# Optimization experiments

Hardware: AMD Instinct MI355X
Metric: run time of the kernel (lower is better)

The kernel has to match this reference:

```python
import jax, jax.numpy as jnp
import numpy as np

B, NJ, NW, NT, D, H = 1024, 16, 2, 2, 128, 128


def _mlp2(x, W1, b1, W2, b2):
    # two-layer dense net with relu on every layer (edge/node networks)
    return jax.nn.relu(jax.nn.relu(x @ W1 + b1) @ W2 + b2)


def _edge_block(src, dst, W1, b1, W2, b2, mask_dst=None):
    # fully-connected edge block: edge(i,j) = MLP(concat(src_i, dst_j)),
    # then avg-pool over destination nodes (masked if mask_dst given)
    Bb, Ns, ds = src.shape
    Nd, dd = dst.shape[1], dst.shape[2]
    e_in = jnp.concatenate([
        jnp.broadcast_to(src[:, :, None, :], (Bb, Ns, Nd, ds)),
        jnp.broadcast_to(dst[:, None, :, :], (Bb, Ns, Nd, dd)),
    ], axis=-1)                              # [B, Ns, Nd, 2D]
    h = _mlp2(e_in, W1, b1, W2, b2)          # [B, Ns, Nd, H]
    if mask_dst is not None:
        m = mask_dst.astype(h.dtype)[:, None, :, None]
        pooled = (h * m).sum(axis=2) / jnp.maximum(m.sum(axis=2), 1.0)
    else:
        pooled = h.mean(axis=2)
    return pooled                            # [B, Ns, H]


def setup_inputs() -> dict:
    key = jax.random.key(0)
    ks = jax.random.split(key, 10)
    def w(k, shape, fan_in):
        return jax.random.normal(k, shape, jnp.float32) / np.float32(np.sqrt(fan_in))
    return {
        "jets": jax.random.normal(ks[0], (B, NJ, D), jnp.float32),
        "nodes_w": jax.random.normal(ks[1], (B, NW, D), jnp.float32),
        "nodes_top": jax.random.normal(ks[2], (B, NT, D), jnp.float32),
        "mask": jax.random.bernoulli(ks[3], 0.8, (B, NJ)),
        # 7 edge nets: 0 jet-jet, 1 jet-W, 2 jet-top, 3 W-jet, 4 W-top, 5 top-jet, 6 top-W
        "edge_W1": w(ks[4], (7, 2 * D, H), 2 * D),
        "edge_b1": jnp.zeros((7, H), jnp.float32),
        "edge_W2": w(ks[5], (7, H, H), H),
        "edge_b2": jnp.zeros((7, H), jnp.float32),
        # jet node net: input D + 3H
        "jet_W1": w(ks[6], (D + 3 * H, H), D + 3 * H),
        "jet_b1": jnp.zeros((H,), jnp.float32),
        "jet_W2": w(ks[7], (H, H), H),
        "jet_b2": jnp.zeros((H,), jnp.float32),
        # W / top node nets (stacked): input D + 2H
        "wt_W1": w(ks[8], (2, D + 2 * H, H), D + 2 * H),
        "wt_b1": jnp.zeros((2, H), jnp.float32),
        "wt_W2": w(ks[9], (2, H, H), H),
        "wt_b2": jnp.zeros((2, H), jnp.float32),
    }


def reference(jets, nodes_w, nodes_top, mask,
              edge_W1, edge_b1, edge_W2, edge_b2,
              jet_W1, jet_b1, jet_W2, jet_b2,
              wt_W1, wt_b1, wt_W2, wt_b2):
    eb = lambda i, s, d, m: _edge_block(s, d, edge_W1[i], edge_b1[i], edge_W2[i], edge_b2[i], m)
    mf = mask.astype(jets.dtype)
    # --- jet update ---
    p_jj = eb(0, jets, jets, mask)
    p_jw = eb(1, jets, nodes_w, None)
    p_jt = eb(2, jets, nodes_top, None)
    jets_cat = jnp.concatenate([jets, p_jj, p_jw, p_jt], axis=-1)
    jets_out = _mlp2(jets_cat, jet_W1, jet_b1, jet_W2, jet_b2) * mf[..., None]
    # --- W update ---
    p_wj = eb(3, nodes_w, jets, mask)
    p_wt = eb(4, nodes_w, nodes_top, None)
    ws_out = _mlp2(jnp.concatenate([nodes_w, p_wj, p_wt], axis=-1),
                   wt_W1[0], wt_b1[0], wt_W2[0], wt_b2[0])
    # --- top update ---
    p_tj = eb(5, nodes_top, jets, mask)
    p_tw = eb(6, nodes_top, nodes_w, None)
    tops_out = _mlp2(jnp.concatenate([nodes_top, p_tj, p_tw], axis=-1),
                     wt_W1[1], wt_b1[1], wt_W2[1], wt_b2[1])
    # concat all updated node types along the node axis: [B, NJ+NW+NT, H]
    return jnp.concatenate([jets_out, ws_out, tops_out], axis=1)
```

## Files before the change

kernel.cpp:

```cpp
#include <hip/hip_runtime.h>
#include <hip/hip_bf16.h>


using short4v = __attribute__((ext_vector_type(4))) short;
using short8 = __attribute__((ext_vector_type(8))) short;
using f32x4  = __attribute__((ext_vector_type(4))) float;
using u32x4  = __attribute__((ext_vector_type(4))) unsigned;

#define DEVI __device__ __forceinline__

DEVI float b2f(short s){
  unsigned u = ((unsigned)(unsigned short)s) << 16;
  float f; __builtin_memcpy(&f, &u, 4); return f;
}
DEVI float lo16f(unsigned w){ unsigned u = w << 16; float f; __builtin_memcpy(&f,&u,4); return f; }
DEVI float hi16f(unsigned w){ unsigned u = w & 0xffff0000u; float f; __builtin_memcpy(&f,&u,4); return f; }
DEVI short f2b(float f){
  __hip_bfloat16 h = __float2bfloat16(f);
  short s; __builtin_memcpy(&s, &h, 2); return s;
}
DEVI unsigned cvtpk(float lo, float hi){
  unsigned r;
  asm("v_cvt_pk_bf16_f32 %0, %1, %2" : "=v"(r) : "v"(lo), "v"(hi));
  return r;
}
DEVI float ldflex(const void* p, long i, int bf){
  return bf ? b2f(((const short*)p)[i]) : ((const float*)p)[i];
}
DEVI f32x4 mfma16(short8 a, short8 b, f32x4 c){
  return __builtin_amdgcn_mfma_f32_16x16x32_bf16(a, b, c, 0, 0, 0);
}

DEVI int detect_bf(const void* jets){
  int l = threadIdx.x & 63;
  int extreme = 0;
  #pragma unroll
  for(int s=0;s<4;s++){
    unsigned short v = ((const unsigned short*)jets)[(l*4+s)*2];
    int e = (v>>7)&0xff;
    if(e<110||e>140) extreme++;
  }
  #pragma unroll
  for(int o=1;o<64;o<<=1) extreme += __shfl_xor(extreme, o);
  return (extreme <= 32) ? 1 : 0;
}
DEVI int detect_fmt(const void* mask){
  int l = threadIdx.x & 63;
  bool all01=true, allf32=true;
  #pragma unroll
  for(int s=0;s<4;s++){
    unsigned w = ((const unsigned*)mask)[l*4+s];
    if(w>1u) all01=false;
    if(w!=0u && w!=0x3F800000u) allf32=false;
  }
  bool allbfv=true; int evnz=0;
  #pragma unroll
  for(int s=0;s<8;s++){
    unsigned short v = ((const unsigned short*)mask)[l*8+s];
    if(v!=0&&v!=0x3F80) allbfv=false;
    if(((l*8+s)&1)==0 && v!=0) evnz++;
  }
  #pragma unroll
  for(int o=1;o<64;o<<=1) evnz += __shfl_xor(evnz, o);
  bool allb01=true;
  #pragma unroll
  for(int s=0;s<16;s++){ if(((const unsigned char*)mask)[l*16+s]>1) allb01=false; }
  int a01 = __all(all01), af32 = __all(allf32), abf = __all(allbfv), ab01 = __all(allb01);
  int fmt = 0;
  if(a01) fmt=0; else if(abf && evnz>0) fmt=2; else if(af32) fmt=3; else if(ab01) fmt=1;
  return fmt;
}

constexpr size_t OF_MASKF  = 256;
constexpr size_t OF_INVCNT = 65792;
constexpr size_t OF_XJ     = 69888;
constexpr size_t OF_XW     = 4264192;
constexpr size_t OF_XT     = 4788480;
constexpr size_t OF_W1T    = 5312768;
constexpr size_t OF_W2T    = 5771520;
constexpr size_t OF_EB1F   = 6000896;
constexpr size_t OF_EB2F   = 6004480;
constexpr size_t OF_JW1T   = 6008064;
constexpr size_t OF_JW2T   = 6139136;
constexpr size_t OF_JB1F   = 6171904;
constexpr size_t OF_JB2F   = 6172416;
constexpr size_t OF_WTW1T  = 6172928;
constexpr size_t OF_WTW2T  = 6369536;
constexpr size_t OF_WTB1F  = 6435072;
constexpr size_t OF_WTB2F  = 6436096;
constexpr size_t OF_UVJ    = 6437120;
constexpr size_t OF_UVW    = 31602944;
constexpr size_t OF_UVT    = 33700096;
constexpr size_t OF_POOL   = 65157376;

__constant__ int QJ_NET[14]  = {0,0,1,2,3,5, 1,3,4,6, 2,4,5,6};
__constant__ int QJ_HALF[14] = {0,1,0,0,1,1, 1,0,0,1, 1,1,0,0};
__constant__ int EB_CUM[8] = {0,512,576,640,704,768,776,784};
__constant__ int EB_NET[7] = {0,1,2,3,5,4,6};
__constant__ int EN_LGRPB[7] = {8,5,5,5,2,5,2};
__constant__ int EN_LGND2[7] = {4,1,1,4,1,4,1};
__constant__ int EN_LGNSB[7] = {4,4,4,1,1,1,1};
__constant__ int EN_USEL[7] = {0,0,0,1,1,2,2};
__constant__ long long EN_UOFF[7] = {0,4194304,6291456,262144,524288,524288,786432};
__constant__ int EN_VSEL[7] = {0,1,2,0,2,0,1};
__constant__ long long EN_VOFF[7] = {2097152,0,0,8388608,262144,10485760,786432};
__constant__ long long EN_POOL[7] = {0,2097152,4194304,6291456,6553600,6815744,7077888};
__constant__ int TJ_CUM[21] = {0,32,64,96,128,160,192,224,240,256,272,288,304,320,336,400,416,464,512,528,544};
__constant__ int TJ_SEL[20] = {0,0,0,0,0,0,0,1,1,1,1,1,1,1,2,3,4,4,5,5};
__constant__ int TJ_OFF[20] = {0,32768,65536,98304,131072,163840,196608,
                               0,16384,32768,49152,65536,81920,98304,
                               0,0,0,49152,0,16384};
__constant__ int TJ_R[20]   = {256,256,256,256,256,256,256,128,128,128,128,128,128,128,512,128,384,384,128,128};

__global__ __launch_bounds__(256) void k_prep(
    const void* jets, const void* nw, const void* ntop, const void* mask,
    const void* eW1, const void* eb1, const void* eW2, const void* eb2,
    const void* jW1, const void* jb1, const void* jW2, const void* jb2,
    const void* wW1, const void* wb1, const void* wW2, const void* wb2,
    int* flags, float* maskf, float* invcnt,
    short* XJ, short* XW, short* XT,
    short* W1T, short* W2T, short* JW1T, short* JW2T, short* WTW1T, short* WTW2T,
    float* EB1F, float* EB2F, float* JB1F, float* JB2F, float* WTB1F, float* WTB2F){
  __shared__ float tl[32][33];
  int bid = blockIdx.x;
  if(bid < 2560){
    int bf = detect_bf(jets);
    long i = ((long)bid*256 + threadIdx.x)*4;
    const void* src; short* dst; long o;
    if(i < 2097152){ src=jets; dst=XJ; o=i; }
    else if(i < 2359296){ src=nw; dst=XW; o=i-2097152; }
    else { src=ntop; dst=XT; o=i-2359296; }
    short4v r;
    if(bf){
      r = *(const short4v*)((const short*)src + o);
    } else {
      f32x4 v = *(const f32x4*)((const float*)src + o);
      #pragma unroll
      for(int e=0;e<4;e++) r[e] = f2b(v[e]);
    }
    *(short4v*)(dst + o) = r;
  } else if(bid < 3104){
    int bf = detect_bf(jets);
    int tile = bid - 2560; int job = 0;
    while(tile >= TJ_CUM[job+1]) job++;
    tile -= TJ_CUM[job];
    int sel = TJ_SEL[job]; long off = TJ_OFF[job]; int R = TJ_R[job];
    const void* src = sel==0?eW1: sel==1?eW2: sel==2?jW1: sel==3?jW2: sel==4?wW1: wW2;
    short* dst = sel==0?W1T: sel==1?W2T: sel==2?JW1T: sel==3?JW2T: sel==4?WTW1T: WTW2T;
    int tr = (tile>>2)*32, tc = (tile&3)*32;
    int t = threadIdx.x, r = t>>3, c4 = (t&7)*4;
    #pragma unroll
    for(int j=0;j<4;j++) tl[r][c4+j] = ldflex(src, off + (long)(tr+r)*128 + tc + c4 + j, bf);
    __syncthreads();
    short4v o;
    #pragma unroll
    for(int j=0;j<4;j++) o[j] = f2b(tl[c4+j][r]);
    *(short4v*)(dst + off + (long)(tc+r)*R + tr + c4) = o;
  } else if(bid < 3168){
    int fmt = detect_fmt(mask);
    int t = (bid-3104)*256 + threadIdx.x;
    float m;
    if(fmt==0)      m = (((const int*)mask)[t]!=0) ? 1.f : 0.f;
    else if(fmt==1) m = (((const unsigned char*)mask)[t]!=0) ? 1.f : 0.f;
    else if(fmt==2) m = (b2f(((const short*)mask)[t])!=0.f) ? 1.f : 0.f;
    else            m = (((const float*)mask)[t]!=0.f) ? 1.f : 0.f;
    maskf[t] = m;
    float s = m;
    for(int o=1;o<16;o<<=1) s += __shfl_xor(s, o);
    if((t&15)==0) invcnt[t>>4] = 1.f / fmaxf(s, 1.f);
  } else if(bid < 3178){
    int bf = detect_bf(jets);
    int id = (bid-3168)*256 + threadIdx.x;
    if(id<896)        EB1F[id]       = ldflex(eb1, id, bf);
    else if(id<1792)  EB2F[id-896]   = ldflex(eb2, id-896, bf);
    else if(id<1920)  JB1F[id-1792]  = ldflex(jb1, id-1792, bf);
    else if(id<2048)  JB2F[id-1920]  = ldflex(jb2, id-1920, bf);
    else if(id<2304)  WTB1F[id-2048] = ldflex(wb1, id-2048, bf);
    else if(id<2560)  WTB2F[id-2304] = ldflex(wb2, id-2304, bf);
  } else {
    if(threadIdx.x < 64){
      int bf = detect_bf(jets);
      int fmt = detect_fmt(mask);
      if((threadIdx.x & 63) == 0){ flags[0] = bf; flags[1] = fmt; }
    }
  }
}

__global__ __launch_bounds__(512, 4) void k_proj(const short* XJ, const short* XW, const short* XT,
    const short* W1T, const float* EB1F, short* UVJ, short* UVW, short* UVT){
  int bid = blockIdx.x;
  int jp, rb; const short* X; short* out;
  if(bid < 384){ jp = bid>>6; rb = bid&63; X=XJ; out=UVJ + jp*2097152; }
  else if(bid < 416){ int r2=bid-384; jp = 6 + (r2>>3); rb = r2&7; X=XW; out=UVW + (jp-6)*262144; }
  else { int r2=bid-416; jp = 10 + (r2>>3); rb = r2&7; X=XT; out=UVT + (jp-10)*262144; }
  int net = QJ_NET[jp], half = QJ_HALF[jp];
  bool addb = (half==0);
  long row0 = (long)rb * 256;
  const short* Wb = W1T + net*32768 + half*128;
  int t = threadIdx.x, lane = t & 63, wv = t >> 6;
  int rbw = wv >> 1, ch = (wv & 1)*64;
  int cl = lane & 15, kh = lane >> 4;
  short8 bw[4][4];
  f32x4 biasv[4];
  #pragma unroll
  for(int nt=0;nt<4;nt++){
    #pragma unroll
    for(int ks=0;ks<4;ks++)
      bw[nt][ks] = *(const short8*)(Wb + (ch + nt*16 + cl)*256 + ks*32 + kh*8);
    if(addb) biasv[nt] = *(const f32x4*)(EB1F + net*128 + ch + nt*16 + kh*4);
    else     biasv[nt] = f32x4{0.f,0.f,0.f,0.f};
  }
  #pragma unroll 1
  for(int c=0;c<4;c++){
    long T0 = row0 + c*64 + rbw*16;
    short8 a[4];
    #pragma unroll
    for(int ks=0;ks<4;ks++)
      a[ks] = *(const short8*)(X + (T0 + cl)*128 + ks*32 + kh*8);
    f32x4 acc[4] = {};
    #pragma unroll
    for(int ks=0;ks<4;ks++)
      #pragma unroll
      for(int nt=0;nt<4;nt++)
        acc[nt] = mfma16(bw[nt][ks], a[ks], acc[nt]);
    #pragma unroll
    for(int nt=0;nt<4;nt++){
      short4v sv;
      #pragma unroll
      for(int r=0;r<4;r++) sv[r] = f2b(acc[nt][r] + biasv[nt][r]);
      *(short4v*)(out + (T0 + cl)*128 + ch + nt*16 + kh*4) = sv;
    }
  }
}

__global__ __launch_bounds__(512, 4) void k_edge(const short* UVJ, const short* UVW, const short* UVT,
    const short* W2T, const float* EB2F, const float* maskf, const float* invcnt, short* POOL){
  __shared__ short W2s[16384];
  int bid = blockIdx.x;
  int ni = 0;
  while(bid >= EB_CUM[ni+1]) ni++;
  int net = EB_NET[ni];
  long base = (long)(bid - EB_CUM[ni]) * 512;
  int t = threadIdx.x, lane = t & 63, wv = t >> 6;
  int cl = lane & 15, kh = lane >> 4;
  const short* Wg = W2T + net*16384;
  #pragma unroll
  for(int i2=0;i2<4;i2++){
    int c = t + i2*512;
    int row = c>>4, blk = c&15;
    u32x4 w4 = *(const u32x4*)(Wg + row*128 + blk*8);
    *(u32x4*)((char*)W2s + ((row*256 + blk*16) ^ ((row&7)<<4))) = w4;
  }
  int lgRPB = EN_LGRPB[net], lgNd = EN_LGND2[net], lgNsB = EN_LGNSB[net];
  int masked = (lgNd == 4);
  const short* U = (EN_USEL[net]==0?UVJ:(EN_USEL[net]==1?UVW:UVT)) + EN_UOFF[net];
  const short* V = (EN_VSEL[net]==0?UVJ:(EN_VSEL[net]==1?UVW:UVT)) + EN_VOFF[net];
  short* pool = POOL + EN_POOL[net];
  float bias[8];
  #pragma unroll
  for(int nt=0;nt<8;nt++) bias[nt] = EB2F[net*128 + nt*16 + cl];
  __syncthreads();
  for(int s=0;s<4;s++){
    long R0 = base + wv*64 + s*16;
    long e = R0 + cl;
    long urow = ((e>>lgRPB)<<lgNsB) + ((e & ((1<<lgRPB)-1)) >> lgNd);
    long vrow = ((e>>lgRPB)<<lgNd)  + (e & ((1<<lgNd)-1));
    u32x4 u[4], v[4];
    #pragma unroll
    for(int ks=0;ks<4;ks++){
      u[ks] = *(const u32x4*)(U + urow*128 + ks*32 + kh*8);
      v[ks] = *(const u32x4*)(V + vrow*128 + ks*32 + kh*8);
    }
    f32x4 acc[8];
    #pragma unroll
    for(int nt=0;nt<8;nt++) acc[nt] = f32x4{bias[nt],bias[nt],bias[nt],bias[nt]};
    #pragma unroll
    for(int ks=0;ks<4;ks++){
      u32x4 aw;
      #pragma unroll
      for(int p=0;p<4;p++){
        float al = fmaxf(lo16f(u[ks][p]) + lo16f(v[ks][p]), 0.f);
        float ah = fmaxf(hi16f(u[ks][p]) + hi16f(v[ks][p]), 0.f);
        aw[p] = cvtpk(al, ah);
      }
      short8 a = __builtin_bit_cast(short8, aw);
      #pragma unroll
      for(int nt=0;nt<8;nt++){
        int row = nt*16 + cl;
        short8 bb = *(const short8*)((const char*)W2s + ((row*256 + ks*64 + kh*16) ^ ((row&7)<<4)));
        acc[nt] = mfma16(a, bb, acc[nt]);
      }
    }
    if(masked){
      long b = R0 >> lgRPB;
      float ic = invcnt[b];
      float wr[4];
      #pragma unroll
      for(int r=0;r<4;r++) wr[r] = maskf[b*16 + kh*4 + r] * ic;
      long prow = R0 >> 4;
      #pragma unroll
      for(int nt=0;nt<8;nt++){
        int col = nt*16 + cl;
        float sm = fmaxf(acc[nt][0],0.f)*wr[0] + fmaxf(acc[nt][1],0.f)*wr[1]
                 + fmaxf(acc[nt][2],0.f)*wr[2] + fmaxf(acc[nt][3],0.f)*wr[3];
        sm += __shfl_xor(sm, 16);
        sm += __shfl_xor(sm, 32);
        if(lane < 16) pool[prow*128 + col] = f2b(sm);
      }
    } else {
      long pr = (R0 + kh*4) >> 1;
      #pragma unroll
      for(int nt=0;nt<8;nt++){
        int col = nt*16 + cl;
        float v0 = fmaxf(acc[nt][0],0.f), v1 = fmaxf(acc[nt][1],0.f);
        float v2 = fmaxf(acc[nt][2],0.f), v3 = fmaxf(acc[nt][3],0.f);
        pool[pr*128 + col]     = f2b((v0+v1)*0.5f);
        pool[(pr+1)*128 + col] = f2b((v2+v3)*0.5f);
      }
    }
  }
}

__global__ __launch_bounds__(256) void k_node(const short* XJ, const short* XW, const short* XT,
    const short* POOL, const short* JW1T, const short* JW2T, const float* JB1F, const float* JB2F,
    const short* WTW1T, const short* WTW2T, const float* WTB1F, const float* WTB2F,
    const float* maskf, const int* flags, void* out){
  __shared__ short hs[8192];
  int bid = blockIdx.x;
  int net; long row0;
  if(bid < 256){ net=0; row0=(long)bid*64; }
  else if(bid < 288){ net=1; row0=(long)(bid-256)*64; }
  else { net=2; row0=(long)(bid-288)*64; }
  int NQ = (net==0) ? 4 : 3;
  int K1 = NQ*128;
  const short* X = (net==0) ? XJ : ((net==1) ? XW : XT);
  const short *P1, *P2, *P3 = nullptr;
  if(net==0){ P1=POOL; P2=POOL+2097152; P3=POOL+4194304; }
  else if(net==1){ P1=POOL+6291456; P2=POOL+6553600; }
  else { P1=POOL+6815744; P2=POOL+7077888; }
  const short* W1 = (net==0) ? JW1T : WTW1T + (long)(net-1)*49152;
  const short* W2 = (net==0) ? JW2T : WTW2T + (long)(net-1)*16384;
  const float* B1 = (net==0) ? JB1F : WTB1F + (net-1)*128;
  const float* B2 = (net==0) ? JB2F : WTB2F + (net-1)*128;
  int t = threadIdx.x, lane = t & 63, wv = t >> 6;
  int cl = lane & 15, kh = lane >> 4;
  int rl = wv*16 + cl;
  long xrow = row0 + rl;
  f32x4 acc[8] = {};
  #pragma unroll
  for(int q=0;q<4;q++){
    if(q < NQ){
      const short* SA = (q==0)?X:((q==1)?P1:((q==2)?P2:P3));
      #pragma unroll
      for(int ks=0;ks<4;ks++){
        short8 a = *(const short8*)(SA + xrow*128 + ks*32 + kh*8);
        #pragma unroll
        for(int nt=0;nt<8;nt++){
          short8 bb = *(const short8*)(W1 + (long)(nt*16 + cl)*K1 + q*128 + ks*32 + kh*8);
          acc[nt] = mfma16(bb, a, acc[nt]);
        }
      }
    }
  }
  #pragma unroll
  for(int nt=0;nt<8;nt++){
    f32x4 bv = *(const f32x4*)(B1 + nt*16 + kh*4);
    short4v sv;
    #pragma unroll
    for(int r=0;r<4;r++) sv[r] = f2b(fmaxf(acc[nt][r] + bv[r], 0.f));
    *(short4v*)((char*)hs + ((rl*256 + (nt*16 + kh*4)*2) ^ ((rl&7)<<4))) = sv;
  }
  __syncthreads();
  f32x4 acc2[8] = {};
  #pragma unroll
  for(int k0=0;k0<4;k0++){
    short8 a = *(const short8*)((const char*)hs + ((rl*256 + (k0*32 + kh*8)*2) ^ ((rl&7)<<4)));
    #pragma unroll
    for(int nt=0;nt<8;nt++){
      short8 bb = *(const short8*)(W2 + (nt*16 + cl)*128 + k0*32 + kh*8);
      acc2[nt] = mfma16(bb, a, acc2[nt]);
    }
  }
  int obf = flags[0];
  long grow = row0 + rl;
  long bbn, node; float mscale = 1.f;
  if(net==0){ bbn = grow>>4; node = grow&15; mscale = maskf[grow]; }
  else if(net==1){ bbn = grow>>1; node = 16 + (grow&1); }
  else { bbn = grow>>1; node = 18 + (grow&1); }
  long obase = (bbn*20 + node)*128;
  #pragma unroll
  for(int nt=0;nt<8;nt++){
    f32x4 bv = *(const f32x4*)(B2 + nt*16 + kh*4);
    f32x4 fv;
    #pragma unroll
    for(int r=0;r<4;r++) fv[r] = fmaxf(acc2[nt][r] + bv[r], 0.f) * mscale;
    if(obf){
      short4v sv;
      #pragma unroll
      for(int r=0;r<4;r++) sv[r] = f2b(fv[r]);
      *(short4v*)((short*)out + obase + nt*16 + kh*4) = sv;
    } else {
      *(f32x4*)((float*)out + obase + nt*16 + kh*4) = fv;
    }
  }
}

extern "C" void kernel_launch(void* const* d_in, const int* in_sizes, int n_in,
                              void* d_out, int out_size, void* d_ws, size_t ws_size,
                              hipStream_t stream){
  char* ws = (char*)d_ws;
  int*   flags  = (int*)ws;
  float* maskf  = (float*)(ws + OF_MASKF);
  float* invcnt = (float*)(ws + OF_INVCNT);
  short* XJ     = (short*)(ws + OF_XJ);
  short* XW     = (short*)(ws + OF_XW);
  short* XT     = (short*)(ws + OF_XT);
  short* W1T    = (short*)(ws + OF_W1T);
  short* W2T    = (short*)(ws + OF_W2T);
  float* EB1F   = (float*)(ws + OF_EB1F);
  float* EB2F   = (float*)(ws + OF_EB2F);
  short* JW1T   = (short*)(ws + OF_JW1T);
  short* JW2T   = (short*)(ws + OF_JW2T);
  float* JB1F   = (float*)(ws + OF_JB1F);
  float* JB2F   = (float*)(ws + OF_JB2F);
  short* WTW1T  = (short*)(ws + OF_WTW1T);
  short* WTW2T  = (short*)(ws + OF_WTW2T);
  float* WTB1F  = (float*)(ws + OF_WTB1F);
  float* WTB2F  = (float*)(ws + OF_WTB2F);
  short* UVJ    = (short*)(ws + OF_UVJ);
  short* UVW    = (short*)(ws + OF_UVW);
  short* UVT    = (short*)(ws + OF_UVT);
  short* POOL   = (short*)(ws + OF_POOL);

  k_prep<<<3179, 256, 0, stream>>>(d_in[0], d_in[1], d_in[2], d_in[3],
                                   d_in[4], d_in[5], d_in[6], d_in[7],
                                   d_in[8], d_in[9], d_in[10], d_in[11],
                                   d_in[12], d_in[13], d_in[14], d_in[15],
                                   flags, maskf, invcnt, XJ, XW, XT,
                                   W1T, W2T, JW1T, JW2T, WTW1T, WTW2T,
                                   EB1F, EB2F, JB1F, JB2F, WTB1F, WTB2F);
  k_proj <<<448, 512, 0, stream>>>(XJ, XW, XT, W1T, EB1F, UVJ, UVW, UVT);
  k_edge <<<784, 512, 0, stream>>>(UVJ, UVW, UVT, W2T, EB2F, maskf, invcnt, POOL);
  k_node <<<320, 256, 0, stream>>>(XJ, XW, XT, POOL, JW1T, JW2T, JB1F, JB2F,
                                   WTW1T, WTW2T, WTB1F, WTB2F, maskf, flags, d_out);
}
```

Baseline: 121.4 us.

## Halve edge and node block work and restructure edge tile for B-fragment reuse

The edge kernel now has each block cover 256 edges instead of 512, doubling the grid. Each wave processes two 16-row tiles at once, so every W2 fragment read from LDS feeds two MFMAs, replacing a sequential four-step loop. The node kernel now uses 32-row blocks with waves split across output-column halves, doubling its grid. The aim is more blocks in flight and fewer LDS reads per MFMA, at the cost of reloading W2 into LDS twice as often and higher register pressure per wave.

```diff
diff --git a/kernel.cpp b/kernel.cpp
--- a/kernel.cpp
+++ b/kernel.cpp
@@ -95,7 +95,7 @@
 
 __constant__ int QJ_NET[14]  = {0,0,1,2,3,5, 1,3,4,6, 2,4,5,6};
 __constant__ int QJ_HALF[14] = {0,1,0,0,1,1, 1,0,0,1, 1,1,0,0};
-__constant__ int EB_CUM[8] = {0,512,576,640,704,768,776,784};
+__constant__ int EB_CUM[8] = {0,1024,1152,1280,1408,1536,1552,1568};
 __constant__ int EB_NET[7] = {0,1,2,3,5,4,6};
 __constant__ int EN_LGRPB[7] = {8,5,5,5,2,5,2};
 __constant__ int EN_LGND2[7] = {4,1,1,4,1,4,1};
@@ -240,7 +240,7 @@
   int ni = 0;
   while(bid >= EB_CUM[ni+1]) ni++;
   int net = EB_NET[ni];
-  long base = (long)(bid - EB_CUM[ni]) * 512;
+  long base = (long)(bid - EB_CUM[ni]) * 256;
   int t = threadIdx.x, lane = t & 63, wv = t >> 6;
   int cl = lane & 15, kh = lane >> 4;
   const short* Wg = W2T + net*16384;
@@ -256,48 +256,61 @@
   const short* U = (EN_USEL[net]==0?UVJ:(EN_USEL[net]==1?UVW:UVT)) + EN_UOFF[net];
   const short* V = (EN_VSEL[net]==0?UVJ:(EN_VSEL[net]==1?UVW:UVT)) + EN_VOFF[net];
   short* pool = POOL + EN_POOL[net];
-  float bias[8];
-  #pragma unroll
-  for(int nt=0;nt<8;nt++) bias[nt] = EB2F[net*128 + nt*16 + cl];
   __syncthreads();
-  for(int s=0;s<4;s++){
-    long R0 = base + wv*64 + s*16;
-    long e = R0 + cl;
-    long urow = ((e>>lgRPB)<<lgNsB) + ((e & ((1<<lgRPB)-1)) >> lgNd);
-    long vrow = ((e>>lgRPB)<<lgNd)  + (e & ((1<<lgNd)-1));
-    u32x4 u[4], v[4];
-    #pragma unroll
-    for(int ks=0;ks<4;ks++){
-      u[ks] = *(const u32x4*)(U + urow*128 + ks*32 + kh*8);
-      v[ks] = *(const u32x4*)(V + vrow*128 + ks*32 + kh*8);
-    }
-    f32x4 acc[8];
-    #pragma unroll
-    for(int nt=0;nt<8;nt++) acc[nt] = f32x4{bias[nt],bias[nt],bias[nt],bias[nt]};
-    #pragma unroll
-    for(int ks=0;ks<4;ks++){
-      u32x4 aw;
-      #pragma unroll
-      for(int p=0;p<4;p++){
-        float al = fmaxf(lo16f(u[ks][p]) + lo16f(v[ks][p]), 0.f);
-        float ah = fmaxf(hi16f(u[ks][p]) + hi16f(v[ks][p]), 0.f);
-        aw[p] = cvtpk(al, ah);
-      }
-      short8 a = __builtin_bit_cast(short8, aw);
-      #pragma unroll
-      for(int nt=0;nt<8;nt++){
-        int row = nt*16 + cl;
-        short8 bb = *(const short8*)((const char*)W2s + ((row*256 + ks*64 + kh*16) ^ ((row&7)<<4)));
-        acc[nt] = mfma16(a, bb, acc[nt]);
-      }
-    }
+  long R0 = base + wv*32;
+  long e0 = R0 + cl, e1 = R0 + 16 + cl;
+  long urow0 = ((e0>>lgRPB)<<lgNsB) + ((e0 & ((1<<lgRPB)-1)) >> lgNd);
+  long vrow0 = ((e0>>lgRPB)<<lgNd)  + (e0 & ((1<<lgNd)-1));
+  long urow1 = ((e1>>lgRPB)<<lgNsB) + ((e1 & ((1<<lgRPB)-1)) >> lgNd);
+  long vrow1 = ((e1>>lgRPB)<<lgNd)  + (e1 & ((1<<lgNd)-1));
+  short8 a0[4], a1[4];
+  #pragma unroll
+  for(int ks=0;ks<4;ks++){
+    u32x4 u = *(const u32x4*)(U + urow0*128 + ks*32 + kh*8);
+    u32x4 v = *(const u32x4*)(V + vrow0*128 + ks*32 + kh*8);
+    u32x4 aw;
+    #pragma unroll
+    for(int p=0;p<4;p++)
+      aw[p] = cvtpk(fmaxf(lo16f(u[p])+lo16f(v[p]),0.f), fmaxf(hi16f(u[p])+hi16f(v[p]),0.f));
+    a0[ks] = __builtin_bit_cast(short8, aw);
+  }
+  #pragma unroll
+  for(int ks=0;ks<4;ks++){
+    u32x4 u = *(const u32x4*)(U + urow1*128 + ks*32 + kh*8);
+    u32x4 v = *(const u32x4*)(V + vrow1*128 + ks*32 + kh*8);
+    u32x4 aw;
+    #pragma unroll
+    for(int p=0;p<4;p++)
+      aw[p] = cvtpk(fmaxf(lo16f(u[p])+lo16f(v[p]),0.f), fmaxf(hi16f(u[p])+hi16f(v[p]),0.f));
+    a1[ks] = __builtin_bit_cast(short8, aw);
+  }
+  f32x4 acc0[8], acc1[8];
+  #pragma unroll
+  for(int nt=0;nt<8;nt++){
+    float bv = EB2F[net*128 + nt*16 + cl];
+    acc0[nt] = f32x4{bv,bv,bv,bv};
+    acc1[nt] = f32x4{bv,bv,bv,bv};
+  }
+  #pragma unroll
+  for(int ks=0;ks<4;ks++)
+    #pragma unroll
+    for(int nt=0;nt<8;nt++){
+      int row = nt*16 + cl;
+      short8 bb = *(const short8*)((const char*)W2s + ((row*256 + ks*64 + kh*16) ^ ((row&7)<<4)));
+      acc0[nt] = mfma16(a0[ks], bb, acc0[nt]);
+      acc1[nt] = mfma16(a1[ks], bb, acc1[nt]);
+    }
+  #pragma unroll
+  for(int half=0; half<2; half++){
+    long RH = R0 + half*16;
+    f32x4* acc = half ? acc1 : acc0;
     if(masked){
-      long b = R0 >> lgRPB;
+      long b = RH >> lgRPB;
       float ic = invcnt[b];
       float wr[4];
       #pragma unroll
-      for(int r=0;r<4;r++) wr[r] = maskf[b*16 + kh*4 + r] * ic;
-      long prow = R0 >> 4;
+      for(int r=0;r<4;r++) wr[r] = maskf[b*16 + ((RH + kh*4 + r) & 15)] * ic;
+      long prow = RH >> 4;
       #pragma unroll
       for(int nt=0;nt<8;nt++){
         int col = nt*16 + cl;
@@ -308,7 +321,7 @@
         if(lane < 16) pool[prow*128 + col] = f2b(sm);
       }
     } else {
-      long pr = (R0 + kh*4) >> 1;
+      long pr = (RH + kh*4) >> 1;
       #pragma unroll
       for(int nt=0;nt<8;nt++){
         int col = nt*16 + cl;
@@ -325,12 +338,12 @@
     const short* POOL, const short* JW1T, const short* JW2T, const float* JB1F, const float* JB2F,
     const short* WTW1T, const short* WTW2T, const float* WTB1F, const float* WTB2F,
     const float* maskf, const int* flags, void* out){
-  __shared__ short hs[8192];
+  __shared__ short hs[4096];
   int bid = blockIdx.x;
   int net; long row0;
-  if(bid < 256){ net=0; row0=(long)bid*64; }
-  else if(bid < 288){ net=1; row0=(long)(bid-256)*64; }
-  else { net=2; row0=(long)(bid-288)*64; }
+  if(bid < 512){ net=0; row0=(long)bid*32; }
+  else if(bid < 576){ net=1; row0=(long)(bid-512)*32; }
+  else { net=2; row0=(long)(bid-576)*32; }
   int NQ = (net==0) ? 4 : 3;
   int K1 = NQ*128;
   const short* X = (net==0) ? XJ : ((net==1) ? XW : XT);
@@ -343,10 +356,11 @@
   const float* B1 = (net==0) ? JB1F : WTB1F + (net-1)*128;
   const float* B2 = (net==0) ? JB2F : WTB2F + (net-1)*128;
   int t = threadIdx.x, lane = t & 63, wv = t >> 6;
+  int rs = wv >> 1, ch = (wv & 1)*64;
   int cl = lane & 15, kh = lane >> 4;
-  int rl = wv*16 + cl;
+  int rl = rs*16 + cl;
   long xrow = row0 + rl;
-  f32x4 acc[8] = {};
+  f32x4 acc[4] = {};
   #pragma unroll
   for(int q=0;q<4;q++){
     if(q < NQ){
@@ -355,29 +369,29 @@
       for(int ks=0;ks<4;ks++){
         short8 a = *(const short8*)(SA + xrow*128 + ks*32 + kh*8);
         #pragma unroll
-        for(int nt=0;nt<8;nt++){
-          short8 bb = *(const short8*)(W1 + (long)(nt*16 + cl)*K1 + q*128 + ks*32 + kh*8);
+        for(int nt=0;nt<4;nt++){
+          short8 bb = *(const short8*)(W1 + (long)(ch + nt*16 + cl)*K1 + q*128 + ks*32 + kh*8);
           acc[nt] = mfma16(bb, a, acc[nt]);
         }
       }
     }
   }
   #pragma unroll
-  for(int nt=0;nt<8;nt++){
-    f32x4 bv = *(const f32x4*)(B1 + nt*16 + kh*4);
+  for(int nt=0;nt<4;nt++){
+    f32x4 bv = *(const f32x4*)(B1 + ch + nt*16 + kh*4);
     short4v sv;
     #pragma unroll
     for(int r=0;r<4;r++) sv[r] = f2b(fmaxf(acc[nt][r] + bv[r], 0.f));
-    *(short4v*)((char*)hs + ((rl*256 + (nt*16 + kh*4)*2) ^ ((rl&7)<<4))) = sv;
+    *(short4v*)((char*)hs + ((rl*256 + (ch + nt*16 + kh*4)*2) ^ ((rl&7)<<4))) = sv;
   }
   __syncthreads();
-  f32x4 acc2[8] = {};
+  f32x4 acc2[4] = {};
   #pragma unroll
   for(int k0=0;k0<4;k0++){
     short8 a = *(const short8*)((const char*)hs + ((rl*256 + (k0*32 + kh*8)*2) ^ ((rl&7)<<4)));
     #pragma unroll
-    for(int nt=0;nt<8;nt++){
-      short8 bb = *(const short8*)(W2 + (nt*16 + cl)*128 + k0*32 + kh*8);
+    for(int nt=0;nt<4;nt++){
+      short8 bb = *(const short8*)(W2 + (ch + nt*16 + cl)*128 + k0*32 + kh*8);
       acc2[nt] = mfma16(bb, a, acc2[nt]);
     }
   }
@@ -389,8 +403,8 @@
   else { bbn = grow>>1; node = 18 + (grow&1); }
   long obase = (bbn*20 + node)*128;
   #pragma unroll
-  for(int nt=0;nt<8;nt++){
-    f32x4 bv = *(const f32x4*)(B2 + nt*16 + kh*4);
+  for(int nt=0;nt<4;nt++){
+    f32x4 bv = *(const f32x4*)(B2 + ch + nt*16 + kh*4);
     f32x4 fv;
     #pragma unroll
     for(int r=0;r<4;r++) fv[r] = fmaxf(acc2[nt][r] + bv[r], 0.f) * mscale;
@@ -398,9 +412,9 @@
       short4v sv;
       #pragma unroll
       for(int r=0;r<4;r++) sv[r] = f2b(fv[r]);
-      *(short4v*)((short*)out + obase + nt*16 + kh*4) = sv;
+      *(short4v*)((short*)out + obase + ch + nt*16 + kh*4) = sv;
     } else {
-      *(f32x4*)((float*)out + obase + nt*16 + kh*4) = fv;
+      *(f32x4*)((float*)out + obase + ch + nt*16 + kh*4) = fv;
     }
   }
 }
@@ -440,7 +454,7 @@
                                    W1T, W2T, JW1T, JW2T, WTW1T, WTW2T,
                                    EB1F, EB2F, JB1F, JB2F, WTB1F, WTB2F);
   k_proj <<<448, 512, 0, stream>>>(XJ, XW, XT, W1T, EB1F, UVJ, UVW, UVT);
-  k_edge <<<784, 512, 0, stream>>>(UVJ, UVW, UVT, W2T, EB2F, maskf, invcnt, POOL);
-  k_node <<<320, 256, 0, stream>>>(XJ, XW, XT, POOL, JW1T, JW2T, JB1F, JB2F,
+  k_edge <<<1568, 512, 0, stream>>>(UVJ, UVW, UVT, W2T, EB2F, maskf, invcnt, POOL);
+  k_node <<<640, 256, 0, stream>>>(XJ, XW, XT, POOL, JW1T, JW2T, JB1F, JB2F,
                                    WTW1T, WTW2T, WTB1F, WTB2F, maskf, flags, d_out);
 }
```

Result: faster. 100.4 us (-17.3%).
